# Kernel optimization log

Measured on AMD Instinct MI355X. Metric: run time of the kernel, lower is better.

Reference implementation:

```python
import jax, jax.numpy as jnp
import numpy as np


def setup_inputs() -> dict:
    key = jax.random.key(0)
    k1, k2, k3, k4 = jax.random.split(key, 4)
    B, H, W, C, NCLS = 128, 14, 14, 512, 200
    # post-ReLU-like non-negative feature map
    x = jax.random.uniform(k1, (B, H, W, C), dtype=jnp.float32)
    # one-hot-like logits for ground-truth labels (only argmax is used)
    gt = jax.random.normal(k2, (B, NCLS), dtype=jnp.float32)
    # positional template codebook; index [H, W] (== shape[0]-1) is the sentinel
    # 'negative' template used for all-zero channels
    t_p = jax.random.normal(k3, (H + 1, W + 1, H, W), dtype=jnp.float32)
    # per-class channel template, broadcast-multiplied with masked features
    class_templates = jax.random.uniform(k4, (NCLS, H, W, C), dtype=jnp.float32)
    return {"x": x, "gt": gt, "t_p": t_p, "class_templates": class_templates}


def reference(x, gt, t_p, class_templates):
    # x: [B, H, W, C] channels-last feature map
    B, H, W, C = x.shape
    flat = x.reshape(B, H * W, C)
    # global spatial argmax per (batch, channel) == max_pool_with_argmax over full extent
    idx = jnp.argmax(flat, axis=1)            # [B, C]
    h = idx // W                               # [B, C]
    w = idx % W                                # [B, C]
    # channels whose spatial max is exactly 0 get the sentinel template index
    empty = jnp.max(flat, axis=1) == 0.0       # [B, C]
    sentinel = t_p.shape[0] - 1
    h = jnp.where(empty, sentinel, h)
    w = jnp.where(empty, sentinel, w)
    # gather positional templates: [B, C, H, W] -> [B, H, W, C]
    templates = jnp.transpose(t_p[h, w], (0, 2, 3, 1))
    masked = jax.nn.relu(x * templates)
    # training branch with gt, reduce_loss=False: mask by the class template
    cls = jnp.argmax(gt, axis=1)               # [B]
    masked = masked * class_templates[cls]     # [B, H, W, C]
    return (masked, x, templates)
```

## Files before the change

kernel.cpp:

```cpp
#include <hip/hip_runtime.h>

#define B    128
#define H    14
#define W    14
#define C    512
#define NCLS 200
#define HW   (H * W)
#define TP_DIM 15
#define SENT_OFF ((14 * TP_DIM + 14) * HW)

typedef float  v4f __attribute__((ext_vector_type(4)));
typedef int    v4i __attribute__((ext_vector_type(4)));

__global__ __launch_bounds__(512) void argmax_kernel(
        const float* __restrict__ x,
        const float* __restrict__ gt,
        int* __restrict__ ws_off,
        int* __restrict__ ws_cls) {
    __shared__ v4f s_best[8][64];
    __shared__ v4i s_idx[8][64];

    const int tid  = threadIdx.x;
    const int b    = blockIdx.x >> 1;
    const int half = blockIdx.x & 1;
    const int cg   = tid & 63;
    const int sl   = tid >> 6;
    const int c0   = half * 256 + cg * 4;

    const int sbeg = sl * 25;
    const int scnt = (sl == 7) ? (HW - 7 * 25) : 25;

    const float* __restrict__ xp = x + (size_t)b * HW * C + c0;

    v4f best = *(const v4f*)(xp + (size_t)sbeg * C);
    v4i bidx = (v4i){sbeg, sbeg, sbeg, sbeg};
#pragma unroll 4
    for (int k = 1; k < scnt; ++k) {
        const int s = sbeg + k;
        v4f v = *(const v4f*)(xp + (size_t)s * C);
        if (v.x > best.x) { best.x = v.x; bidx.x = s; }
        if (v.y > best.y) { best.y = v.y; bidx.y = s; }
        if (v.z > best.z) { best.z = v.z; bidx.z = s; }
        if (v.w > best.w) { best.w = v.w; bidx.w = s; }
    }
    s_best[sl][cg] = best;
    s_idx[sl][cg]  = bidx;
    __syncthreads();

    if (tid < 64) {
        v4f cb = s_best[0][tid];
        v4i ci = s_idx[0][tid];
#pragma unroll
        for (int k = 1; k < 8; ++k) {
            v4f p = s_best[k][tid];
            v4i q = s_idx[k][tid];
            if (p.x > cb.x) { cb.x = p.x; ci.x = q.x; }
            if (p.y > cb.y) { cb.y = p.y; ci.y = q.y; }
            if (p.z > cb.z) { cb.z = p.z; ci.z = q.z; }
            if (p.w > cb.w) { cb.w = p.w; ci.w = q.w; }
        }
        v4i o;
        o.x = (cb.x == 0.0f) ? SENT_OFF : ((ci.x / W) * TP_DIM + (ci.x % W)) * HW;
        o.y = (cb.y == 0.0f) ? SENT_OFF : ((ci.y / W) * TP_DIM + (ci.y % W)) * HW;
        o.z = (cb.z == 0.0f) ? SENT_OFF : ((ci.z / W) * TP_DIM + (ci.z % W)) * HW;
        o.w = (cb.w == 0.0f) ? SENT_OFF : ((ci.w / W) * TP_DIM + (ci.w % W)) * HW;
        *(v4i*)(ws_off + (size_t)b * C + half * 256 + tid * 4) = o;
    } else if (half == 0 && tid < 128) {
        const int lane = tid - 64;
        const float* __restrict__ g = gt + (size_t)b * NCLS;
        float gb = -__builtin_inff();
        int   gi = NCLS;
        for (int i = lane; i < NCLS; i += 64) {
            float v = g[i];
            if (v > gb) { gb = v; gi = i; }
        }
#pragma unroll
        for (int d = 1; d < 64; d <<= 1) {
            float ov = __shfl_xor(gb, d);
            int   oi = __shfl_xor(gi, d);
            if (ov > gb || (ov == gb && oi < gi)) { gb = ov; gi = oi; }
        }
        if (lane == 0) ws_cls[b] = gi;
    }
}

__global__ __launch_bounds__(256) void stream_kernel(
        const float* __restrict__ x,
        const float* __restrict__ t_p,
        const float* __restrict__ ctpl,
        const int*   __restrict__ ws_off,
        const int*   __restrict__ ws_cls,
        float*       __restrict__ out) {
    const int b     = blockIdx.x & 127;
    const int chunk = blockIdx.x >> 7;
    const int cls   = ws_cls[b];

    const size_t plane = (size_t)B * HW * C;
    const int*   __restrict__ offp = ws_off + (size_t)b * C;
    const float* __restrict__ ctp  = ctpl + (size_t)cls * HW * C;

    for (int t = chunk * 256 + (int)threadIdx.x; t < 49 * 128; t += 2048) {
        const int q  = t >> 7;
        const int cg = t & 127;
        const int s0 = q * 4;
        const int c0 = cg * 4;

        v4i off = *(const v4i*)(offp + c0);

        v4f t0 = *(const v4f*)(t_p + off.x + s0);
        v4f t1 = *(const v4f*)(t_p + off.y + s0);
        v4f t2 = *(const v4f*)(t_p + off.z + s0);
        v4f t3 = *(const v4f*)(t_p + off.w + s0);
        v4f tv[4];
        tv[0] = (v4f){t0.x, t1.x, t2.x, t3.x};
        tv[1] = (v4f){t0.y, t1.y, t2.y, t3.y};
        tv[2] = (v4f){t0.z, t1.z, t2.z, t3.z};
        tv[3] = (v4f){t0.w, t1.w, t2.w, t3.w};

        const size_t base = ((size_t)b * HW + s0) * C + c0;
        const float* __restrict__ xp = x + base;
        const float* __restrict__ cp = ctp + (size_t)s0 * C + c0;
        float* __restrict__ out_m = out + base;
        float* __restrict__ out_x = out + plane + base;
        float* __restrict__ out_t = out + 2 * plane + base;

#pragma unroll
        for (int i = 0; i < 4; ++i) {
            v4f xv = *(const v4f*)(xp + (size_t)i * C);
            v4f ct = *(const v4f*)(cp + (size_t)i * C);
            v4f tt = tv[i];
            v4f m;
            m.x = fmaxf(xv.x * tt.x, 0.0f) * ct.x;
            m.y = fmaxf(xv.y * tt.y, 0.0f) * ct.y;
            m.z = fmaxf(xv.z * tt.z, 0.0f) * ct.z;
            m.w = fmaxf(xv.w * tt.w, 0.0f) * ct.w;
            __builtin_nontemporal_store(m,  (v4f*)(out_m + (size_t)i * C));
            __builtin_nontemporal_store(xv, (v4f*)(out_x + (size_t)i * C));
            __builtin_nontemporal_store(tt, (v4f*)(out_t + (size_t)i * C));
        }
    }
}

extern "C" void kernel_launch(void* const* d_in, const int* in_sizes, int n_in,
                              void* d_out, int out_size, void* d_ws, size_t ws_size,
                              hipStream_t stream) {
    const float* x    = (const float*)d_in[0];
    const float* gt   = (const float*)d_in[1];
    const float* t_p  = (const float*)d_in[2];
    const float* ctpl = (const float*)d_in[3];
    float* out = (float*)d_out;

    int* ws_off = (int*)d_ws;
    int* ws_cls = ws_off + B * C;

    hipLaunchKernelGGL(argmax_kernel,
                       dim3(2 * B), dim3(512), 0, stream,
                       x, gt, ws_off, ws_cls);
    hipLaunchKernelGGL(stream_kernel,
                       dim3(8 * B), dim3(256), 0, stream,
                       x, t_p, ctpl, ws_off, ws_cls, out);
}
```

Baseline: 272.4 us.

## Fuse argmax and streaming kernels into one per-batch-half kernel

Merges the argmax pass and the streaming output pass into one kernel, so each block computes the template offsets and class index in shared memory and then writes its half of the channels for one batch. The spatial scan now runs on 7 of the 8 wavefronts. The eighth computes the gt argmax at the same time. This removes a kernel launch and the global workspace round trip, and lets the second pass reread x while it is likely still in cache. In exchange the grid drops from 1024 to 256 blocks for the bandwidth-bound streaming phase, which may lower memory-level parallelism on a GPU with many CUs.

```diff
diff --git a/kernel.cpp b/kernel.cpp
--- a/kernel.cpp
+++ b/kernel.cpp
@@ -12,13 +12,16 @@
 typedef float  v4f __attribute__((ext_vector_type(4)));
 typedef int    v4i __attribute__((ext_vector_type(4)));
 
-__global__ __launch_bounds__(512) void argmax_kernel(
+__global__ __launch_bounds__(512) void fused_kernel(
         const float* __restrict__ x,
         const float* __restrict__ gt,
-        int* __restrict__ ws_off,
-        int* __restrict__ ws_cls) {
-    __shared__ v4f s_best[8][64];
-    __shared__ v4i s_idx[8][64];
+        const float* __restrict__ t_p,
+        const float* __restrict__ ctpl,
+        float*       __restrict__ out) {
+    __shared__ v4f s_best[7][64];
+    __shared__ v4i s_idx[7][64];
+    __shared__ int s_off[256];
+    __shared__ int s_cls;
 
     const int tid  = threadIdx.x;
     const int b    = blockIdx.x >> 1;
@@ -27,46 +30,25 @@
     const int sl   = tid >> 6;
     const int c0   = half * 256 + cg * 4;
 
-    const int sbeg = sl * 25;
-    const int scnt = (sl == 7) ? (HW - 7 * 25) : 25;
-
     const float* __restrict__ xp = x + (size_t)b * HW * C + c0;
 
-    v4f best = *(const v4f*)(xp + (size_t)sbeg * C);
-    v4i bidx = (v4i){sbeg, sbeg, sbeg, sbeg};
-#pragma unroll 4
-    for (int k = 1; k < scnt; ++k) {
-        const int s = sbeg + k;
-        v4f v = *(const v4f*)(xp + (size_t)s * C);
-        if (v.x > best.x) { best.x = v.x; bidx.x = s; }
-        if (v.y > best.y) { best.y = v.y; bidx.y = s; }
-        if (v.z > best.z) { best.z = v.z; bidx.z = s; }
-        if (v.w > best.w) { best.w = v.w; bidx.w = s; }
-    }
-    s_best[sl][cg] = best;
-    s_idx[sl][cg]  = bidx;
-    __syncthreads();
-
-    if (tid < 64) {
-        v4f cb = s_best[0][tid];
-        v4i ci = s_idx[0][tid];
-#pragma unroll
-        for (int k = 1; k < 8; ++k) {
-            v4f p = s_best[k][tid];
-            v4i q = s_idx[k][tid];
-            if (p.x > cb.x) { cb.x = p.x; ci.x = q.x; }
-            if (p.y > cb.y) { cb.y = p.y; ci.y = q.y; }
-            if (p.z > cb.z) { cb.z = p.z; ci.z = q.z; }
-            if (p.w > cb.w) { cb.w = p.w; ci.w = q.w; }
+    if (sl < 7) {
+        const int sbeg = sl * 28;
+        v4f best = *(const v4f*)(xp + (size_t)sbeg * C);
+        v4i bidx = (v4i){sbeg, sbeg, sbeg, sbeg};
+#pragma unroll 9
+        for (int k = 1; k < 28; ++k) {
+            const int s = sbeg + k;
+            v4f v = *(const v4f*)(xp + (size_t)s * C);
+            if (v.x > best.x) { best.x = v.x; bidx.x = s; }
+            if (v.y > best.y) { best.y = v.y; bidx.y = s; }
+            if (v.z > best.z) { best.z = v.z; bidx.z = s; }
+            if (v.w > best.w) { best.w = v.w; bidx.w = s; }
         }
-        v4i o;
-        o.x = (cb.x == 0.0f) ? SENT_OFF : ((ci.x / W) * TP_DIM + (ci.x % W)) * HW;
-        o.y = (cb.y == 0.0f) ? SENT_OFF : ((ci.y / W) * TP_DIM + (ci.y % W)) * HW;
-        o.z = (cb.z == 0.0f) ? SENT_OFF : ((ci.z / W) * TP_DIM + (ci.z % W)) * HW;
-        o.w = (cb.w == 0.0f) ? SENT_OFF : ((ci.w / W) * TP_DIM + (ci.w % W)) * HW;
-        *(v4i*)(ws_off + (size_t)b * C + half * 256 + tid * 4) = o;
-    } else if (half == 0 && tid < 128) {
-        const int lane = tid - 64;
+        s_best[sl][cg] = best;
+        s_idx[sl][cg]  = bidx;
+    } else {
+        const int lane = cg;
         const float* __restrict__ g = gt + (size_t)b * NCLS;
         float gb = -__builtin_inff();
         int   gi = NCLS;
@@ -80,32 +62,39 @@
             int   oi = __shfl_xor(gi, d);
             if (ov > gb || (ov == gb && oi < gi)) { gb = ov; gi = oi; }
         }
-        if (lane == 0) ws_cls[b] = gi;
+        if (lane == 0) s_cls = gi;
     }
-}
+    __syncthreads();
 
-__global__ __launch_bounds__(256) void stream_kernel(
-        const float* __restrict__ x,
-        const float* __restrict__ t_p,
-        const float* __restrict__ ctpl,
-        const int*   __restrict__ ws_off,
-        const int*   __restrict__ ws_cls,
-        float*       __restrict__ out) {
-    const int b     = blockIdx.x & 127;
-    const int chunk = blockIdx.x >> 7;
-    const int cls   = ws_cls[b];
+    if (tid < 64) {
+        v4f cb = s_best[0][tid];
+        v4i ci = s_idx[0][tid];
+#pragma unroll
+        for (int k = 1; k < 7; ++k) {
+            v4f p = s_best[k][tid];
+            v4i q = s_idx[k][tid];
+            if (p.x > cb.x) { cb.x = p.x; ci.x = q.x; }
+            if (p.y > cb.y) { cb.y = p.y; ci.y = q.y; }
+            if (p.z > cb.z) { cb.z = p.z; ci.z = q.z; }
+            if (p.w > cb.w) { cb.w = p.w; ci.w = q.w; }
+        }
+        v4i o;
+        o.x = (cb.x == 0.0f) ? SENT_OFF : ((ci.x / W) * TP_DIM + (ci.x % W)) * HW;
+        o.y = (cb.y == 0.0f) ? SENT_OFF : ((ci.y / W) * TP_DIM + (ci.y % W)) * HW;
+        o.z = (cb.z == 0.0f) ? SENT_OFF : ((ci.z / W) * TP_DIM + (ci.z % W)) * HW;
+        o.w = (cb.w == 0.0f) ? SENT_OFF : ((ci.w / W) * TP_DIM + (ci.w % W)) * HW;
+        *(v4i*)&s_off[tid * 4] = o;
+    }
+    __syncthreads();
+
+    const int klass = s_cls;
+    const v4i off   = *(const v4i*)&s_off[cg * 4];
 
     const size_t plane = (size_t)B * HW * C;
-    const int*   __restrict__ offp = ws_off + (size_t)b * C;
-    const float* __restrict__ ctp  = ctpl + (size_t)cls * HW * C;
+    const float* __restrict__ ctp = ctpl + (size_t)klass * HW * C;
 
-    for (int t = chunk * 256 + (int)threadIdx.x; t < 49 * 128; t += 2048) {
-        const int q  = t >> 7;
-        const int cg = t & 127;
+    for (int q = sl; q < 49; q += 8) {
         const int s0 = q * 4;
-        const int c0 = cg * 4;
-
-        v4i off = *(const v4i*)(offp + c0);
 
         v4f t0 = *(const v4f*)(t_p + off.x + s0);
         v4f t1 = *(const v4f*)(t_p + off.y + s0);
@@ -118,7 +107,7 @@
         tv[3] = (v4f){t0.w, t1.w, t2.w, t3.w};
 
         const size_t base = ((size_t)b * HW + s0) * C + c0;
-        const float* __restrict__ xp = x + base;
+        const float* __restrict__ xq = x + base;
         const float* __restrict__ cp = ctp + (size_t)s0 * C + c0;
         float* __restrict__ out_m = out + base;
         float* __restrict__ out_x = out + plane + base;
@@ -126,7 +115,7 @@
 
 #pragma unroll
         for (int i = 0; i < 4; ++i) {
-            v4f xv = *(const v4f*)(xp + (size_t)i * C);
+            v4f xv = *(const v4f*)(xq + (size_t)i * C);
             v4f ct = *(const v4f*)(cp + (size_t)i * C);
             v4f tt = tv[i];
             v4f m;
@@ -150,13 +139,7 @@
     const float* ctpl = (const float*)d_in[3];
     float* out = (float*)d_out;
 
-    int* ws_off = (int*)d_ws;
-    int* ws_cls = ws_off + B * C;
-
-    hipLaunchKernelGGL(argmax_kernel,
+    hipLaunchKernelGGL(fused_kernel,
                        dim3(2 * B), dim3(512), 0, stream,
-                       x, gt, ws_off, ws_cls);
-    hipLaunchKernelGGL(stream_kernel,
-                       dim3(8 * B), dim3(256), 0, stream,
-                       x, t_p, ctpl, ws_off, ws_cls, out);
+                       x, gt, t_p, ctpl, out);
 }
```

New measurement: 260.6 us. -4.4%, faster.
